# Kernel optimization log

Measured on AMD Instinct MI355X. Metric: run time of the kernel, lower is better.

## Reference

```python
import jax, jax.numpy as jnp
import numpy as np

D_MODEL = 1024
D_FF = 4096
BATCH = 4
SEQ = 4096
DILATION = 1


def _dw_causal_conv(x, w, dilation):
    # x: [B, S, D], w: [D, 1, K] (depthwise, torch Conv1d groups=D layout)
    k = w.shape[-1]
    pad = (k - 1) * dilation
    h = jnp.transpose(x, (0, 2, 1))  # [B, D, S]
    out = jax.lax.conv_general_dilated(
        h, w,
        window_strides=(1,),
        padding=[(pad, 0)],  # causal left pad
        rhs_dilation=(dilation,),
        dimension_numbers=('NCH', 'OIH', 'NCH'),
        feature_group_count=h.shape[1],
    )
    return jnp.transpose(out, (0, 2, 1))  # [B, S, D]


def _rmsnorm(x, w):
    ms = jnp.mean(jnp.square(x), axis=-1, keepdims=True)
    return x * jax.lax.rsqrt(ms + 1e-6) * w


def setup_inputs() -> dict:
    key = jax.random.key(0)
    ks = jax.random.split(key, 12)
    s = lambda d: 1.0 / np.sqrt(d)
    return {
        'x': jax.random.normal(ks[0], (BATCH, SEQ, D_MODEL), jnp.float32),
        'ln1_w': jnp.ones((D_MODEL,), jnp.float32),
        'ln2_w': jnp.ones((D_MODEL,), jnp.float32),
        'w_fine': jax.random.normal(ks[1], (D_MODEL, 1, 3), jnp.float32) * 0.5,
        'w_medium': jax.random.normal(ks[2], (D_MODEL, 1, 5), jnp.float32) * 0.4,
        'w_coarse': jax.random.normal(ks[3], (D_MODEL, 1, 7), jnp.float32) * 0.3,
        'sg_w': jax.random.normal(ks[4], (3, D_MODEL), jnp.float32) * 0.02,
        'up_w': jax.random.normal(ks[5], (2 * D_MODEL, D_MODEL), jnp.float32) * s(D_MODEL),
        'down_w': jax.random.normal(ks[6], (D_MODEL, D_MODEL), jnp.float32) * s(D_MODEL),
        'wg': jax.random.normal(ks[7], (D_FF, D_MODEL), jnp.float32) * s(D_MODEL),
        'wu': jax.random.normal(ks[8], (D_FF, D_MODEL), jnp.float32) * s(D_MODEL),
        'wo': jax.random.normal(ks[9], (D_MODEL, D_FF), jnp.float32) * s(D_FF),
    }


def reference(x, ln1_w, ln2_w, w_fine, w_medium, w_coarse, sg_w, up_w, down_w, wg, wu, wo):
    # --- MSAC mixer with pre-norm residual ---
    h = _rmsnorm(x, ln1_w)
    gv = jnp.einsum('bsd,ed->bse', h, up_w)        # [B, S, 2D]
    gate, val = jnp.split(gv, 2, axis=-1)
    gate = jax.nn.sigmoid(gate)
    c_fine = _dw_causal_conv(val, w_fine, DILATION)
    c_medium = _dw_causal_conv(val, w_medium, DILATION)
    c_coarse = _dw_causal_conv(val, w_coarse, DILATION)
    scale_w = jax.nn.softmax(jnp.einsum('bsd,ed->bse', h, sg_w), axis=-1)  # [B, S, 3]
    fused = (scale_w[..., 0:1] * c_fine
             + scale_w[..., 1:2] * c_medium
             + scale_w[..., 2:3] * c_coarse)
    x = x + jnp.einsum('bsd,ed->bse', fused * gate, down_w)
    # --- SwiGLU FFN with pre-norm residual ---
    h2 = _rmsnorm(x, ln2_w)
    g = jax.nn.silu(jnp.einsum('bsd,fd->bsf', h2, wg))
    u = jnp.einsum('bsd,fd->bsf', h2, wu)
    x = x + jnp.einsum('bsf,df->bsd', g * u, wo)
    return x
```

## Files before the change

### kernel.cpp

```cpp
#include <hip/hip_runtime.h>
#include <stdint.h>

#define D_MODEL 1024
#define D_FF    4096
#define NTOK    16384
#define SEQ     4096

typedef __bf16 bf16x8 __attribute__((ext_vector_type(8)));
typedef float  f32x4  __attribute__((ext_vector_type(4)));

typedef __attribute__((address_space(1))) void gvoid;
typedef __attribute__((address_space(3))) void svoid;

__device__ __forceinline__ unsigned short f2bf(float f) {
  union { float f; uint32_t u; } v; v.f = f;
  uint32_t u = v.u;
  u += 0x7FFFu + ((u >> 16) & 1u);
  return (unsigned short)(u >> 16);
}
__device__ __forceinline__ float bf2f(unsigned short h) {
  union { uint32_t u; float f; } v; v.u = ((uint32_t)h) << 16;
  return v.f;
}

__device__ __forceinline__ void gload16(const void* g, void* l) {
  __builtin_amdgcn_global_load_lds((gvoid*)g, (svoid*)l, 16, 0, 0);
}

__device__ __forceinline__ float fast_sigmoid(float x) {
  return __builtin_amdgcn_rcpf(1.f + __expf(-x));
}

__global__ __launch_bounds__(256) void cvt_k(const float* __restrict__ S,
                                             unsigned short* __restrict__ D, int n4) {
  int i = blockIdx.x * 256 + threadIdx.x;
  if (i < n4) {
    float4 f = reinterpret_cast<const float4*>(S)[i];
    ushort4 o;
    o.x = f2bf(f.x); o.y = f2bf(f.y); o.z = f2bf(f.z); o.w = f2bf(f.w);
    reinterpret_cast<ushort4*>(D)[i] = o;
  }
}

__global__ __launch_bounds__(256) void cvt_il_k(const float* __restrict__ G,
                                                const float* __restrict__ U,
                                                unsigned short* __restrict__ D) {
  int i = blockIdx.x * 256 + threadIdx.x;
  const int row = i >> 8;
  const int c4  = i & 255;
  const float* src = ((row & 1) ? U : G) + (size_t)(row >> 1) * 1024 + c4 * 4;
  float4 f = *reinterpret_cast<const float4*>(src);
  ushort4 o;
  o.x = f2bf(f.x); o.y = f2bf(f.y); o.z = f2bf(f.z); o.w = f2bf(f.w);
  reinterpret_cast<ushort4*>(D)[i] = o;
}

template<bool SG>
__global__ __launch_bounds__(256) void rmsnorm_k(
    const float* __restrict__ X, const float* __restrict__ W,
    const float* __restrict__ SGW,
    unsigned short* __restrict__ H, float* __restrict__ SCL)
{
  const int n = blockIdx.x;
  const int t = threadIdx.x;
  float4 x = reinterpret_cast<const float4*>(X + (size_t)n * D_MODEL)[t];
  float4 w = reinterpret_cast<const float4*>(W)[t];
  float4 hw;
  hw.x = x.x * w.x; hw.y = x.y * w.y; hw.z = x.z * w.z; hw.w = x.w * w.w;
  float ss = x.x*x.x + x.y*x.y + x.z*x.z + x.w*x.w;
  float p0 = 0.f, p1 = 0.f, p2 = 0.f;
  if (SG) {
    float4 s0 = reinterpret_cast<const float4*>(SGW)[t];
    float4 s1 = reinterpret_cast<const float4*>(SGW + D_MODEL)[t];
    float4 s2 = reinterpret_cast<const float4*>(SGW + 2 * D_MODEL)[t];
    p0 = hw.x*s0.x + hw.y*s0.y + hw.z*s0.z + hw.w*s0.w;
    p1 = hw.x*s1.x + hw.y*s1.y + hw.z*s1.z + hw.w*s1.w;
    p2 = hw.x*s2.x + hw.y*s2.y + hw.z*s2.z + hw.w*s2.w;
  }
  #pragma unroll
  for (int off = 32; off > 0; off >>= 1) {
    ss += __shfl_xor(ss, off);
    if (SG) {
      p0 += __shfl_xor(p0, off);
      p1 += __shfl_xor(p1, off);
      p2 += __shfl_xor(p2, off);
    }
  }
  __shared__ float red[4][4];
  const int wid = t >> 6;
  if ((t & 63) == 0) { red[wid][0] = ss; red[wid][1] = p0; red[wid][2] = p1; red[wid][3] = p2; }
  __syncthreads();
  ss = red[0][0] + red[1][0] + red[2][0] + red[3][0];
  const float r = rsqrtf(ss * (1.0f / D_MODEL) + 1e-6f);
  ushort4 h4;
  h4.x = f2bf(hw.x * r); h4.y = f2bf(hw.y * r); h4.z = f2bf(hw.z * r); h4.w = f2bf(hw.w * r);
  reinterpret_cast<ushort4*>(H + (size_t)n * D_MODEL)[t] = h4;
  if (SG && t == 0) {
    float l0 = (red[0][1] + red[1][1] + red[2][1] + red[3][1]) * r;
    float l1 = (red[0][2] + red[1][2] + red[2][2] + red[3][2]) * r;
    float l2 = (red[0][3] + red[1][3] + red[2][3] + red[3][3]) * r;
    float mx = fmaxf(l0, fmaxf(l1, l2));
    float e0 = expf(l0 - mx), e1 = expf(l1 - mx), e2 = expf(l2 - mx);
    float inv = 1.f / (e0 + e1 + e2);
    SCL[n * 3 + 0] = e0 * inv; SCL[n * 3 + 1] = e1 * inv; SCL[n * 3 + 2] = e2 * inv;
  }
}

__global__ __launch_bounds__(256) void conv_k(
    const unsigned short* __restrict__ GV,
    const float* __restrict__ SCL,
    const float* __restrict__ W3, const float* __restrict__ W5, const float* __restrict__ W7,
    unsigned short* __restrict__ Y)
{
  const int n = blockIdx.x;
  const int t = threadIdx.x;
  const int d0 = t * 4;
  const int s = n & (SEQ - 1);
  const unsigned short* vbase = GV + (size_t)n * (2 * D_MODEL) + D_MODEL + d0;
  float v[7][4];
  #pragma unroll
  for (int j = 0; j < 7; ++j) {
    const int tap = 6 - j;
    if (tap <= s) {
      ushort4 u = *reinterpret_cast<const ushort4*>(vbase - (size_t)tap * (2 * D_MODEL));
      v[j][0] = bf2f(u.x); v[j][1] = bf2f(u.y); v[j][2] = bf2f(u.z); v[j][3] = bf2f(u.w);
    } else {
      v[j][0] = 0.f; v[j][1] = 0.f; v[j][2] = 0.f; v[j][3] = 0.f;
    }
  }
  ushort4 gb = *reinterpret_cast<const ushort4*>(GV + (size_t)n * (2 * D_MODEL) + d0);
  float gf[4] = { bf2f(gb.x), bf2f(gb.y), bf2f(gb.z), bf2f(gb.w) };
  const float sc0 = SCL[n * 3 + 0], sc1 = SCL[n * 3 + 1], sc2 = SCL[n * 3 + 2];
  ushort4 out;
  unsigned short o[4];
  #pragma unroll
  for (int i = 0; i < 4; ++i) {
    const int d = d0 + i;
    float c3 = W3[d*3+0]*v[4][i] + W3[d*3+1]*v[5][i] + W3[d*3+2]*v[6][i];
    float c5 = W5[d*5+0]*v[2][i] + W5[d*5+1]*v[3][i] + W5[d*5+2]*v[4][i]
             + W5[d*5+3]*v[5][i] + W5[d*5+4]*v[6][i];
    float c7 = 0.f;
    #pragma unroll
    for (int j = 0; j < 7; ++j) c7 += W7[d*7+j] * v[j][i];
    const float g = fast_sigmoid(gf[i]);
    o[i] = f2bf((sc0 * c3 + sc1 * c5 + sc2 * c7) * g);
  }
  out.x = o[0]; out.y = o[1]; out.z = o[2]; out.w = o[3];
  reinterpret_cast<ushort4*>(Y + (size_t)n * D_MODEL)[t] = out;
}


#define EPI_BF16      0
#define EPI_RES       1
#define EPI_SWIGLU_IL 2

#define STAGE_A(tt, h) do { if ((tt) < nt) { \
    char* d_ = dstBase + (((tt)&1) << 16) + ((h) << 14); \
    const unsigned short* s_ = aSrc + (size_t)((h)*128) * K + (tt)*64; \
    gload16(s_, d_); gload16(s_ + (size_t)64 * K, d_ + 8192); } } while(0)

#define STAGE_B(tt, h) do { if ((tt) < nt) { \
    char* d_ = dstBase + (((tt)&1) << 16) + 32768 + ((h) << 14); \
    const unsigned short* s_ = bSrc + (size_t)((h)*32) * K + (tt)*64; \
    gload16(s_, d_); gload16(s_ + (size_t)128 * K, d_ + 8192); } } while(0)

#define STAGE_A2(tt) do { STAGE_A(tt, 0); STAGE_A(tt, 1); } while(0)

#define DSR(dst, base, IMM) \
  asm volatile("ds_read_b128 %0, %1 offset:" #IMM : "=v"(dst) : "v"(base))

#define LOAD_AQ0(S) do { \
  DSR(aq[0][0], aA##S##k0, 0);    DSR(aq[0][1], aA##S##k1, 0); \
  DSR(aq[1][0], aA##S##k0, 2048); DSR(aq[1][1], aA##S##k1, 2048); \
  DSR(aq[2][0], aA##S##k0, 4096); DSR(aq[2][1], aA##S##k1, 4096); \
  DSR(aq[3][0], aA##S##k0, 6144); DSR(aq[3][1], aA##S##k1, 6144); } while(0)

#define LOAD_AQ1(S) do { \
  DSR(aq[0][0], aA##S##k0, 8192);  DSR(aq[0][1], aA##S##k1, 8192); \
  DSR(aq[1][0], aA##S##k0, 10240); DSR(aq[1][1], aA##S##k1, 10240); \
  DSR(aq[2][0], aA##S##k0, 12288); DSR(aq[2][1], aA##S##k1, 12288); \
  DSR(aq[3][0], aA##S##k0, 14336); DSR(aq[3][1], aA##S##k1, 14336); } while(0)

#define LOAD_B_H0(S) do { \
  DSR(b0[0][0], bB##S##k0, 0);    DSR(b0[0][1], bB##S##k1, 0); \
  DSR(b0[1][0], bB##S##k0, 2048); DSR(b0[1][1], bB##S##k1, 2048); } while(0)

#define LOAD_B_H1(S) do { \
  DSR(b1[0][0], bB##S##k0, 16384); DSR(b1[0][1], bB##S##k1, 16384); \
  DSR(b1[1][0], bB##S##k0, 18432); DSR(b1[1][1], bB##S##k1, 18432); } while(0)

#define MMAQ(BR, MQ, NQ) do { \
  _Pragma("unroll") for (int f_ = 0; f_ < 4; ++f_) \
  _Pragma("unroll") for (int e_ = 0; e_ < 2; ++e_) { \
    acc[(MQ)*4+f_][(NQ)*2+e_] = __builtin_amdgcn_mfma_f32_16x16x32_bf16( \
        aq[f_][0], BR[e_][0], acc[(MQ)*4+f_][(NQ)*2+e_], 0, 0, 0); \
    acc[(MQ)*4+f_][(NQ)*2+e_] = __builtin_amdgcn_mfma_f32_16x16x32_bf16( \
        aq[f_][1], BR[e_][1], acc[(MQ)*4+f_][(NQ)*2+e_], 0, 0, 0); \
  } } while(0)

#define THROTTLE8 asm volatile("s_waitcnt lgkmcnt(8)" ::: "memory")

#define PH_MID() \
  __builtin_amdgcn_s_barrier(); \
  asm volatile("s_waitcnt lgkmcnt(0)" ::: "memory"); \
  __builtin_amdgcn_sched_barrier(0); \
  __builtin_amdgcn_s_setprio(1)

#define PHASE_END() \
  __builtin_amdgcn_s_setprio(0); \
  __builtin_amdgcn_s_barrier()

#define PHASE_END_VM() \
  __builtin_amdgcn_s_setprio(0); \
  asm volatile("s_waitcnt vmcnt(6)" ::: "memory"); \
  __builtin_amdgcn_s_barrier()

#define PHASE_END_VM0() \
  __builtin_amdgcn_s_setprio(0); \
  asm volatile("s_waitcnt vmcnt(0)" ::: "memory"); \
  __builtin_amdgcn_s_barrier()

template<int EPI>
__global__ __launch_bounds__(512, 2) void gemm256_k(
    const unsigned short* __restrict__ A,
    const unsigned short* __restrict__ B0g,
    const float* __restrict__ RES,
    void* __restrict__ OUT,
    int M, int N, int K)
{
  __shared__ uint4 lds4[8192];
  char* lbase = (char*)lds4;

  const int tid  = threadIdx.x;
  const int lane = tid & 63;
  const int wid  = tid >> 6;
  const int wm   = wid >> 2;
  const int wn   = wid & 3;
  const int l15 = lane & 15, l4 = lane >> 4, l7 = lane & 7;
  const int m0 = blockIdx.x * 256;
  const int n0 = blockIdx.y * 256;
  const int nt = K >> 6;

  const int r0 = tid >> 3;
  const int kc = (tid & 7) ^ (r0 & 7);
  const unsigned short* aSrc = A + (size_t)(m0 + r0) * K + kc * 8;
  const unsigned short* bSrc = B0g + (size_t)(n0 + (r0 >> 5) * 64 + (r0 & 31)) * K + kc * 8;
  char* dstBase = lbase + tid * 16;

  const unsigned colswz = (unsigned)((l4 ^ l7) << 4);
  const unsigned aA0k0 = (unsigned)((wm << 14) + l15 * 128) + colswz;
  const unsigned aA0k1 = aA0k0 ^ 0x40u;
  const unsigned aA1k0 = aA0k0 + 65536u;
  const unsigned aA1k1 = aA0k1 + 65536u;
  const unsigned bB0k0 = (unsigned)(32768 + (wn * 32 + l15) * 128) + colswz;
  const unsigned bB0k1 = bB0k0 ^ 0x40u;
  const unsigned bB1k0 = bB0k0 + 65536u;
  const unsigned bB1k1 = bB0k1 + 65536u;

  f32x4 acc[8][4];
  #pragma unroll
  for (int i = 0; i < 8; ++i)
    #pragma unroll
    for (int j = 0; j < 4; ++j)
      #pragma unroll
      for (int r = 0; r < 4; ++r) acc[i][j][r] = 0.f;

  bf16x8 aq[4][2], b0[2][2], b1[2][2];

  STAGE_A(0, 0); STAGE_A(0, 1); STAGE_B(0, 0); STAGE_B(0, 1);
  STAGE_A(1, 0); STAGE_A(1, 1); STAGE_B(1, 1);
  asm volatile("s_waitcnt vmcnt(6)" ::: "memory");
  __builtin_amdgcn_s_barrier();

  for (int t = 0; t + 2 < nt; t += 2) {
    LOAD_AQ0(0); LOAD_B_H0(0);
    STAGE_B(t + 1, 0);
    THROTTLE8;
    PH_MID(); MMAQ(b0, 0, 0); PHASE_END();
    LOAD_B_H1(0);
    PH_MID(); MMAQ(b1, 0, 1); PHASE_END();
    LOAD_AQ1(0);
    STAGE_B(t + 2, 1);
    PH_MID(); MMAQ(b1, 1, 1); PHASE_END();
    STAGE_A2(t + 2);
    PH_MID(); MMAQ(b0, 1, 0); PHASE_END_VM();
    LOAD_AQ0(1); LOAD_B_H0(1);
    STAGE_B(t + 2, 0);
    THROTTLE8;
    PH_MID(); MMAQ(b0, 0, 0); PHASE_END();
    LOAD_B_H1(1);
    PH_MID(); MMAQ(b1, 0, 1); PHASE_END();
    LOAD_AQ1(1);
    STAGE_B(t + 3, 1);
    PH_MID(); MMAQ(b1, 1, 1); PHASE_END();
    STAGE_A2(t + 3);
    PH_MID(); MMAQ(b0, 1, 0); PHASE_END_VM();
  }

  {
    LOAD_AQ0(0); LOAD_B_H0(0);
    STAGE_B(nt - 1, 0);
    THROTTLE8;
    PH_MID(); MMAQ(b0, 0, 0); PHASE_END();
    LOAD_B_H1(0);
    PH_MID(); MMAQ(b1, 0, 1); PHASE_END();
    LOAD_AQ1(0);
    PH_MID(); MMAQ(b1, 1, 1); PHASE_END();
    PH_MID(); MMAQ(b0, 1, 0); PHASE_END_VM0();
    LOAD_AQ0(1); LOAD_B_H0(1);
    THROTTLE8;
    PH_MID(); MMAQ(b0, 0, 0); PHASE_END();
    LOAD_B_H1(1);
    PH_MID(); MMAQ(b1, 0, 1); PHASE_END();
    LOAD_AQ1(1);
    PH_MID(); MMAQ(b1, 1, 1); PHASE_END();
    PH_MID(); MMAQ(b0, 1, 0); PHASE_END();
  }

  if (M < -1) ((float*)OUT)[tid] = ((float*)lds4)[tid];

  const int cr = (lane >> 4) * 4;
  const int cc = lane & 15;
  #pragma unroll
  for (int F = 0; F < 8; ++F)
    #pragma unroll
    for (int E = 0; E < 4; ++E)
      #pragma unroll
      for (int rr = 0; rr < 4; ++rr) {
        const int grow = m0 + wm * 128 + (F >> 2) * 64 + (F & 3) * 16 + cr + rr;
        const int gcol = n0 + wn * 64 + (E >> 1) * 32 + (E & 1) * 16 + cc;
        const float v = acc[F][E][rr];
        if (EPI == EPI_BF16) {
          ((unsigned short*)OUT)[(size_t)grow * N + gcol] = f2bf(v);
        } else if (EPI == EPI_RES) {
          const size_t idx = (size_t)grow * N + gcol;
          ((float*)OUT)[idx] = RES[idx] + v;
        } else {
          const float pv = __shfl_xor(v, 1);
          const float g = (cc & 1) ? pv : v;
          const float u = (cc & 1) ? v : pv;
          const float o = g * fast_sigmoid(g) * u;
          unsigned int ob = f2bf(o);
          const unsigned int o2 = __shfl_xor((int)ob, 2);
          if ((cc & 3) == 0) {
            const int ff = gcol >> 1;
            *reinterpret_cast<unsigned int*>(
                &((unsigned short*)OUT)[(size_t)grow * (D_FF) + ff]) = ob | (o2 << 16);
          }
        }
      }
}

extern "C" void kernel_launch(void* const* d_in, const int* in_sizes, int n_in,
                              void* d_out, int out_size, void* d_ws, size_t ws_size,
                              hipStream_t stream)
{
  const float* x    = (const float*)d_in[0];
  const float* ln1w = (const float*)d_in[1];
  const float* ln2w = (const float*)d_in[2];
  const float* wf   = (const float*)d_in[3];
  const float* wm   = (const float*)d_in[4];
  const float* wco  = (const float*)d_in[5];
  const float* sgw  = (const float*)d_in[6];
  const float* upw  = (const float*)d_in[7];
  const float* dnw  = (const float*)d_in[8];
  const float* wg   = (const float*)d_in[9];
  const float* wu   = (const float*)d_in[10];
  const float* wo   = (const float*)d_in[11];

  char* ws = (char*)d_ws;
  size_t off = 0;
  auto alloc = [&](size_t bytes) -> void* {
    void* p = ws + off;
    off += (bytes + 255) & ~(size_t)255;
    return p;
  };
  unsigned short* wb_up = (unsigned short*)alloc((size_t)2048 * 1024 * 2);
  unsigned short* wb_dn = (unsigned short*)alloc((size_t)1024 * 1024 * 2);
  unsigned short* wb_il = (unsigned short*)alloc((size_t)8192 * 1024 * 2);
  unsigned short* wb_wo = (unsigned short*)alloc((size_t)1024 * 4096 * 2);
  float*          scl   = (float*)alloc((size_t)NTOK * 3 * 4);
  unsigned short* h2b   = (unsigned short*)alloc((size_t)NTOK * D_MODEL * 2);
  char* big = (char*)alloc((size_t)NTOK * 4096 * 2);
  unsigned short* hb  = (unsigned short*)big;
  unsigned short* gvb = (unsigned short*)(big + (size_t)NTOK * 1024 * 2);
  unsigned short* yb  = (unsigned short*)(big + (size_t)NTOK * 3072 * 2);
  unsigned short* gub = (unsigned short*)big;
  float* x1 = (float*)d_out;

  cvt_k<<<2048, 256, 0, stream>>>(upw, wb_up, 2048 * 1024 / 4);
  cvt_k<<<1024, 256, 0, stream>>>(dnw, wb_dn, 1024 * 1024 / 4);
  cvt_il_k<<<8192, 256, 0, stream>>>(wg, wu, wb_il);
  cvt_k<<<4096, 256, 0, stream>>>(wo, wb_wo, 1024 * 4096 / 4);

  rmsnorm_k<true><<<NTOK, 256, 0, stream>>>(x, ln1w, sgw, hb, scl);
  gemm256_k<EPI_BF16><<<dim3(64, 8), 512, 0, stream>>>(hb, wb_up, nullptr, gvb, NTOK, 2048, 1024);
  conv_k<<<NTOK, 256, 0, stream>>>(gvb, scl, wf, wm, wco, yb);
  gemm256_k<EPI_RES><<<dim3(64, 4), 512, 0, stream>>>(yb, wb_dn, x, x1, NTOK, 1024, 1024);
  rmsnorm_k<false><<<NTOK, 256, 0, stream>>>(x1, ln2w, nullptr, h2b, nullptr);
  gemm256_k<EPI_SWIGLU_IL><<<dim3(64, 32), 512, 0, stream>>>(h2b, wb_il, nullptr, gub, NTOK, 8192, 1024);
  gemm256_k<EPI_RES><<<dim3(64, 4), 512, 0, stream>>>(gub, wb_wo, x1, (float*)d_out, NTOK, 1024, 4096);
}
```

Baseline: 767.4 us.

## Restructure GEMM main loop pipeline, add block swizzle, regroup SwiGLU interleave

Rewrites the GEMM K-loop schedule. There are fewer barriers per step, partial lgkmcnt gates let MFMAs start before all LDS reads land, and A/B tile prefetches are reordered with vmcnt(4) waits. It adds an XCD-aware block-index swizzle to improve L2 locality across chiplets. The gate/up weight interleave changes from per-row to 16-row groups, so the SwiGLU epilogue reads g and u from adjacent accumulators without lane shuffles. The new wait counts and stage ordering are easy to get wrong and could introduce races or stalls.

```diff
diff --git a/kernel.cpp b/kernel.cpp
--- a/kernel.cpp
+++ b/kernel.cpp
@@ -48,7 +48,9 @@
   int i = blockIdx.x * 256 + threadIdx.x;
   const int row = i >> 8;
   const int c4  = i & 255;
-  const float* src = ((row & 1) ? U : G) + (size_t)(row >> 1) * 1024 + c4 * 4;
+  const int gi = row >> 5, w = row & 31;
+  const float* src = (w < 16 ? G + (size_t)(gi * 16 + w) * 1024
+                             : U + (size_t)(gi * 16 + (w - 16)) * 1024) + c4 * 4;
   float4 f = *reinterpret_cast<const float4*>(src);
   ushort4 o;
   o.x = f2bf(f.x); o.y = f2bf(f.y); o.z = f2bf(f.z); o.w = f2bf(f.w);
@@ -154,40 +156,40 @@
 #define EPI_RES       1
 #define EPI_SWIGLU_IL 2
 
-#define STAGE_A(tt, h) do { if ((tt) < nt) { \
+#define STAGE_A(tt, h) do { \
     char* d_ = dstBase + (((tt)&1) << 16) + ((h) << 14); \
     const unsigned short* s_ = aSrc + (size_t)((h)*128) * K + (tt)*64; \
-    gload16(s_, d_); gload16(s_ + (size_t)64 * K, d_ + 8192); } } while(0)
-
-#define STAGE_B(tt, h) do { if ((tt) < nt) { \
+    gload16(s_, d_); gload16(s_ + (size_t)64 * K, d_ + 8192); } while(0)
+
+#define STAGE_B(tt, h) do { \
     char* d_ = dstBase + (((tt)&1) << 16) + 32768 + ((h) << 14); \
     const unsigned short* s_ = bSrc + (size_t)((h)*32) * K + (tt)*64; \
-    gload16(s_, d_); gload16(s_ + (size_t)128 * K, d_ + 8192); } } while(0)
-
-#define STAGE_A2(tt) do { STAGE_A(tt, 0); STAGE_A(tt, 1); } while(0)
+    gload16(s_, d_); gload16(s_ + (size_t)128 * K, d_ + 8192); } while(0)
 
 #define DSR(dst, base, IMM) \
   asm volatile("ds_read_b128 %0, %1 offset:" #IMM : "=v"(dst) : "v"(base))
 
-#define LOAD_AQ0(S) do { \
+#define RD_B0(S) do { \
+  DSR(b0[0][0], bB##S##k0, 0);    DSR(b0[0][1], bB##S##k1, 0); \
+  DSR(b0[1][0], bB##S##k0, 2048); DSR(b0[1][1], bB##S##k1, 2048); } while(0)
+
+#define RD_B1(S) do { \
+  DSR(b1[0][0], bB##S##k0, 16384); DSR(b1[0][1], bB##S##k1, 16384); \
+  DSR(b1[1][0], bB##S##k0, 18432); DSR(b1[1][1], bB##S##k1, 18432); } while(0)
+
+#define RD_AQ0(S) do { \
   DSR(aq[0][0], aA##S##k0, 0);    DSR(aq[0][1], aA##S##k1, 0); \
   DSR(aq[1][0], aA##S##k0, 2048); DSR(aq[1][1], aA##S##k1, 2048); \
   DSR(aq[2][0], aA##S##k0, 4096); DSR(aq[2][1], aA##S##k1, 4096); \
   DSR(aq[3][0], aA##S##k0, 6144); DSR(aq[3][1], aA##S##k1, 6144); } while(0)
 
-#define LOAD_AQ1(S) do { \
+#define RD_AQ1A(S) do { \
   DSR(aq[0][0], aA##S##k0, 8192);  DSR(aq[0][1], aA##S##k1, 8192); \
-  DSR(aq[1][0], aA##S##k0, 10240); DSR(aq[1][1], aA##S##k1, 10240); \
+  DSR(aq[1][0], aA##S##k0, 10240); DSR(aq[1][1], aA##S##k1, 10240); } while(0)
+
+#define RD_AQ1B(S) do { \
   DSR(aq[2][0], aA##S##k0, 12288); DSR(aq[2][1], aA##S##k1, 12288); \
   DSR(aq[3][0], aA##S##k0, 14336); DSR(aq[3][1], aA##S##k1, 14336); } while(0)
-
-#define LOAD_B_H0(S) do { \
-  DSR(b0[0][0], bB##S##k0, 0);    DSR(b0[0][1], bB##S##k1, 0); \
-  DSR(b0[1][0], bB##S##k0, 2048); DSR(b0[1][1], bB##S##k1, 2048); } while(0)
-
-#define LOAD_B_H1(S) do { \
-  DSR(b1[0][0], bB##S##k0, 16384); DSR(b1[0][1], bB##S##k1, 16384); \
-  DSR(b1[1][0], bB##S##k0, 18432); DSR(b1[1][1], bB##S##k1, 18432); } while(0)
 
 #define MMAQ(BR, MQ, NQ) do { \
   _Pragma("unroll") for (int f_ = 0; f_ < 4; ++f_) \
@@ -198,27 +200,24 @@
         aq[f_][1], BR[e_][1], acc[(MQ)*4+f_][(NQ)*2+e_], 0, 0, 0); \
   } } while(0)
 
-#define THROTTLE8 asm volatile("s_waitcnt lgkmcnt(8)" ::: "memory")
-
-#define PH_MID() \
-  __builtin_amdgcn_s_barrier(); \
-  asm volatile("s_waitcnt lgkmcnt(0)" ::: "memory"); \
-  __builtin_amdgcn_sched_barrier(0); \
-  __builtin_amdgcn_s_setprio(1)
-
-#define PHASE_END() \
-  __builtin_amdgcn_s_setprio(0); \
-  __builtin_amdgcn_s_barrier()
-
-#define PHASE_END_VM() \
-  __builtin_amdgcn_s_setprio(0); \
-  asm volatile("s_waitcnt vmcnt(6)" ::: "memory"); \
-  __builtin_amdgcn_s_barrier()
-
-#define PHASE_END_VM0() \
-  __builtin_amdgcn_s_setprio(0); \
-  asm volatile("s_waitcnt vmcnt(0)" ::: "memory"); \
-  __builtin_amdgcn_s_barrier()
+#define MMAQH(BR, MQ, NQ, F0) do { \
+  _Pragma("unroll") for (int f_ = (F0); f_ < (F0) + 2; ++f_) \
+  _Pragma("unroll") for (int e_ = 0; e_ < 2; ++e_) { \
+    acc[(MQ)*4+f_][(NQ)*2+e_] = __builtin_amdgcn_mfma_f32_16x16x32_bf16( \
+        aq[f_][0], BR[e_][0], acc[(MQ)*4+f_][(NQ)*2+e_], 0, 0, 0); \
+    acc[(MQ)*4+f_][(NQ)*2+e_] = __builtin_amdgcn_mfma_f32_16x16x32_bf16( \
+        aq[f_][1], BR[e_][1], acc[(MQ)*4+f_][(NQ)*2+e_], 0, 0, 0); \
+  } } while(0)
+
+#define GATE4 do { asm volatile("s_waitcnt lgkmcnt(4)" ::: "memory"); \
+                   __builtin_amdgcn_sched_barrier(0); } while(0)
+#define GATE0 do { asm volatile("s_waitcnt lgkmcnt(0)" ::: "memory"); \
+                   __builtin_amdgcn_sched_barrier(0); } while(0)
+#define VM4   asm volatile("s_waitcnt vmcnt(4)" ::: "memory")
+#define VM0   asm volatile("s_waitcnt vmcnt(0)" ::: "memory")
+#define BAR   __builtin_amdgcn_s_barrier()
+#define PRIO1 __builtin_amdgcn_s_setprio(1)
+#define PRIO0 __builtin_amdgcn_s_setprio(0)
 
 template<int EPI>
 __global__ __launch_bounds__(512, 2) void gemm256_k(
@@ -237,8 +236,13 @@
   const int wm   = wid >> 2;
   const int wn   = wid & 3;
   const int l15 = lane & 15, l4 = lane >> 4, l7 = lane & 7;
-  const int m0 = blockIdx.x * 256;
-  const int n0 = blockIdx.y * 256;
+
+  const int nbx = gridDim.x;
+  const int id  = blockIdx.y * nbx + blockIdx.x;
+  const int cpx = (nbx * gridDim.y) >> 3;
+  const int swz = (id & 7) * cpx + (id >> 3);
+  const int m0 = (swz % nbx) * 256;
+  const int n0 = (swz / nbx) * 256;
   const int nt = K >> 6;
 
   const int r0 = tid >> 3;
@@ -268,87 +272,92 @@
   bf16x8 aq[4][2], b0[2][2], b1[2][2];
 
   STAGE_A(0, 0); STAGE_A(0, 1); STAGE_B(0, 0); STAGE_B(0, 1);
-  STAGE_A(1, 0); STAGE_A(1, 1); STAGE_B(1, 1);
-  asm volatile("s_waitcnt vmcnt(6)" ::: "memory");
-  __builtin_amdgcn_s_barrier();
+  STAGE_B(1, 0); STAGE_B(1, 1);
+  VM4;
+  BAR;
 
   for (int t = 0; t + 2 < nt; t += 2) {
-    LOAD_AQ0(0); LOAD_B_H0(0);
-    STAGE_B(t + 1, 0);
-    THROTTLE8;
-    PH_MID(); MMAQ(b0, 0, 0); PHASE_END();
-    LOAD_B_H1(0);
-    PH_MID(); MMAQ(b1, 0, 1); PHASE_END();
-    LOAD_AQ1(0);
-    STAGE_B(t + 2, 1);
-    PH_MID(); MMAQ(b1, 1, 1); PHASE_END();
-    STAGE_A2(t + 2);
-    PH_MID(); MMAQ(b0, 1, 0); PHASE_END_VM();
-    LOAD_AQ0(1); LOAD_B_H0(1);
-    STAGE_B(t + 2, 0);
-    THROTTLE8;
-    PH_MID(); MMAQ(b0, 0, 0); PHASE_END();
-    LOAD_B_H1(1);
-    PH_MID(); MMAQ(b1, 0, 1); PHASE_END();
-    LOAD_AQ1(1);
-    STAGE_B(t + 3, 1);
-    PH_MID(); MMAQ(b1, 1, 1); PHASE_END();
-    STAGE_A2(t + 3);
-    PH_MID(); MMAQ(b0, 1, 0); PHASE_END_VM();
+    RD_B0(0); RD_AQ0(0); RD_B1(0);
+    STAGE_A(t + 1, 0); STAGE_A(t + 1, 1);
+    GATE4; PRIO1; MMAQ(b0, 0, 0); PRIO0;
+    GATE0; PRIO1; MMAQ(b1, 0, 1); PRIO0;
+    BAR;
+    RD_AQ1A(0); RD_AQ1B(0);
+    STAGE_B(t + 2, 0); STAGE_B(t + 2, 1);
+    GATE4; PRIO1; MMAQH(b1, 1, 1, 0); MMAQH(b0, 1, 0, 0); PRIO0;
+    GATE0; PRIO1; MMAQH(b1, 1, 1, 2); MMAQH(b0, 1, 0, 2); PRIO0;
+    VM4;
+    BAR;
+    RD_B0(1); RD_AQ0(1); RD_B1(1);
+    STAGE_A(t + 2, 0); STAGE_A(t + 2, 1);
+    GATE4; PRIO1; MMAQ(b0, 0, 0); PRIO0;
+    GATE0; PRIO1; MMAQ(b1, 0, 1); PRIO0;
+    BAR;
+    RD_AQ1A(1); RD_AQ1B(1);
+    STAGE_B(t + 3, 0); STAGE_B(t + 3, 1);
+    GATE4; PRIO1; MMAQH(b1, 1, 1, 0); MMAQH(b0, 1, 0, 0); PRIO0;
+    GATE0; PRIO1; MMAQH(b1, 1, 1, 2); MMAQH(b0, 1, 0, 2); PRIO0;
+    VM4;
+    BAR;
   }
 
   {
-    LOAD_AQ0(0); LOAD_B_H0(0);
-    STAGE_B(nt - 1, 0);
-    THROTTLE8;
-    PH_MID(); MMAQ(b0, 0, 0); PHASE_END();
-    LOAD_B_H1(0);
-    PH_MID(); MMAQ(b1, 0, 1); PHASE_END();
-    LOAD_AQ1(0);
-    PH_MID(); MMAQ(b1, 1, 1); PHASE_END();
-    PH_MID(); MMAQ(b0, 1, 0); PHASE_END_VM0();
-    LOAD_AQ0(1); LOAD_B_H0(1);
-    THROTTLE8;
-    PH_MID(); MMAQ(b0, 0, 0); PHASE_END();
-    LOAD_B_H1(1);
-    PH_MID(); MMAQ(b1, 0, 1); PHASE_END();
-    LOAD_AQ1(1);
-    PH_MID(); MMAQ(b1, 1, 1); PHASE_END();
-    PH_MID(); MMAQ(b0, 1, 0); PHASE_END();
+    RD_B0(0); RD_AQ0(0); RD_B1(0);
+    STAGE_A(nt - 1, 0); STAGE_A(nt - 1, 1);
+    GATE4; PRIO1; MMAQ(b0, 0, 0); PRIO0;
+    GATE0; PRIO1; MMAQ(b1, 0, 1); PRIO0;
+    BAR;
+    RD_AQ1A(0); RD_AQ1B(0);
+    GATE4; PRIO1; MMAQH(b1, 1, 1, 0); MMAQH(b0, 1, 0, 0); PRIO0;
+    GATE0; PRIO1; MMAQH(b1, 1, 1, 2); MMAQH(b0, 1, 0, 2); PRIO0;
+    VM0;
+    BAR;
+    RD_B0(1); RD_AQ0(1); RD_B1(1);
+    GATE4; PRIO1; MMAQ(b0, 0, 0); PRIO0;
+    GATE0; PRIO1; MMAQ(b1, 0, 1); PRIO0;
+    BAR;
+    RD_AQ1A(1); RD_AQ1B(1);
+    GATE4; PRIO1; MMAQH(b1, 1, 1, 0); MMAQH(b0, 1, 0, 0); PRIO0;
+    GATE0; PRIO1; MMAQH(b1, 1, 1, 2); MMAQH(b0, 1, 0, 2); PRIO0;
+    BAR;
   }
 
   if (M < -1) ((float*)OUT)[tid] = ((float*)lds4)[tid];
 
   const int cr = (lane >> 4) * 4;
   const int cc = lane & 15;
-  #pragma unroll
-  for (int F = 0; F < 8; ++F)
+  if (EPI == EPI_SWIGLU_IL) {
+    const int ffbase = (n0 + wn * 64) >> 1;
     #pragma unroll
-    for (int E = 0; E < 4; ++E)
+    for (int F = 0; F < 8; ++F)
       #pragma unroll
-      for (int rr = 0; rr < 4; ++rr) {
-        const int grow = m0 + wm * 128 + (F >> 2) * 64 + (F & 3) * 16 + cr + rr;
-        const int gcol = n0 + wn * 64 + (E >> 1) * 32 + (E & 1) * 16 + cc;
-        const float v = acc[F][E][rr];
-        if (EPI == EPI_BF16) {
-          ((unsigned short*)OUT)[(size_t)grow * N + gcol] = f2bf(v);
-        } else if (EPI == EPI_RES) {
-          const size_t idx = (size_t)grow * N + gcol;
-          ((float*)OUT)[idx] = RES[idx] + v;
-        } else {
-          const float pv = __shfl_xor(v, 1);
-          const float g = (cc & 1) ? pv : v;
-          const float u = (cc & 1) ? v : pv;
+      for (int p = 0; p < 2; ++p)
+        #pragma unroll
+        for (int rr = 0; rr < 4; ++rr) {
+          const int grow = m0 + wm * 128 + (F >> 2) * 64 + (F & 3) * 16 + cr + rr;
+          const float g = acc[F][2 * p][rr];
+          const float u = acc[F][2 * p + 1][rr];
           const float o = g * fast_sigmoid(g) * u;
-          unsigned int ob = f2bf(o);
-          const unsigned int o2 = __shfl_xor((int)ob, 2);
-          if ((cc & 3) == 0) {
-            const int ff = gcol >> 1;
-            *reinterpret_cast<unsigned int*>(
-                &((unsigned short*)OUT)[(size_t)grow * (D_FF) + ff]) = ob | (o2 << 16);
+          ((unsigned short*)OUT)[(size_t)grow * D_FF + ffbase + p * 16 + cc] = f2bf(o);
+        }
+  } else {
+    #pragma unroll
+    for (int F = 0; F < 8; ++F)
+      #pragma unroll
+      for (int E = 0; E < 4; ++E)
+        #pragma unroll
+        for (int rr = 0; rr < 4; ++rr) {
+          const int grow = m0 + wm * 128 + (F >> 2) * 64 + (F & 3) * 16 + cr + rr;
+          const int gcol = n0 + wn * 64 + (E >> 1) * 32 + (E & 1) * 16 + cc;
+          const float v = acc[F][E][rr];
+          if (EPI == EPI_BF16) {
+            ((unsigned short*)OUT)[(size_t)grow * N + gcol] = f2bf(v);
+          } else {
+            const size_t idx = (size_t)grow * N + gcol;
+            ((float*)OUT)[idx] = RES[idx] + v;
           }
         }
-      }
+  }
 }
 
 extern "C" void kernel_launch(void* const* d_in, const int* in_sizes, int n_in,
```

Measured after the change: 683.9 us. 10.9% less time.
